# Performance work log

Hardware: AMD Instinct MI355X
Metric: run time of the kernel (lower is better)

## Reference

```python
import jax, jax.numpy as jnp
from jax import lax
import numpy as np

MAX_ATOMS = 50
MAX_DEGREE = 4
MAX_RINGS = 16
BATCH = 16384
EDGE_KEEP_PROB = 0.3  # fraction of neighbor slots that are real edges; rest are -1 (masked)


def setup_inputs() -> dict:
    key = jax.random.key(0)
    k1, k2 = jax.random.split(key)
    e = jax.random.randint(k1, (BATCH, MAX_ATOMS, MAX_DEGREE), 0, MAX_ATOMS, dtype=jnp.int32)
    keep = jax.random.uniform(k2, (BATCH, MAX_ATOMS, MAX_DEGREE)) < EDGE_KEEP_PROB
    edge = jnp.where(keep, e, jnp.int32(-1))
    return {"edge": edge}


def reference(edge):
    B, A, D = edge.shape
    N = A + 1  # node 0 is the masked-edge sentinel after +1 shift and zero-row pad
    bidx = jnp.arange(B)
    # masked_edges: shift indices by +1, pad a zero row at atom index 0 -> [B, N, D]
    me = jnp.pad(edge.astype(jnp.int32) + 1, ((0, 0), (1, 0), (0, 0)))

    # per-node state, shape [B, N]
    lnf = jnp.ones((B, N), jnp.int32).at[:, 0].set(0).at[:, 1].set(0)  # leaf_not_found
    nnv = jnp.ones((B, N), jnp.int32).at[:, 0].set(0)                  # node_not_visited
    Tree = jnp.zeros((B, N), jnp.int32)                                 # parent pointers
    num_rings = jnp.zeros((B,), jnp.int32)
    ring_idx = jnp.zeros((B, N, 2), jnp.int32)

    def visit(state, visiting):
        lnf, nnv, Tree, num_rings, ring_idx = state
        for d in range(D):  # small static degree loop (4)
            nxt = me[bidx, visiting, d]                 # [B]
            slnf = lnf[bidx, nxt]                       # specific_leaf_not_found
            slnv = nnv[bidx, nxt]                       # specific_leaf_not_visited
            cyc = (1 - slnf) * slnv * (nxt != 0).astype(jnp.int32)  # cycle_found
            ring_idx = ring_idx.at[bidx, num_rings, 0].add(visiting * cyc)
            ring_idx = ring_idx.at[bidx, num_rings, 1].add(nxt * cyc)
            num_rings = num_rings + cyc
            Tree = Tree.at[bidx, nxt].add(slnf * visiting)
            lnf = lnf.at[bidx, nxt].set(0)
        nnv = nnv.at[bidx, visiting].set(0)
        return (lnf, nnv, Tree, num_rings, ring_idx)

    # atom_idx == 1: visit node 1 (special-cased init above)
    state = visit((lnf, nnv, Tree, num_rings, ring_idx), jnp.ones((B,), jnp.int32))

    def atom_body(_, state):
        lnf, nnv = state[0], state[1]
        visiting = jnp.argmax(nnv * (1 - lnf), axis=-1).astype(jnp.int32)
        return visit(state, visiting)

    state = lax.fori_loop(2, A + 1, atom_body, state)
    lnf, nnv, Tree, num_rings, ring_idx = state

    max_num_rings = jnp.max(num_rings)
    rings = jnp.zeros((B, MAX_RINGS, A), jnp.int32)

    def ring_body(carry):
        i, rings = carry
        air = jnp.zeros((B,), jnp.int32)  # atom_in_ring_idx

        # branch 0: mark ancestor chain of ring endpoint 0
        start = ring_idx[:, i, 0]
        vb0 = jnp.zeros((B, N), jnp.int32).at[bidx, start].set(1)
        def mark0(_, c):
            vb0, start = c
            nxt = Tree[bidx, start]
            return (vb0.at[bidx, nxt].set(1), nxt)
        vb0, _ = lax.fori_loop(0, A, mark0, (vb0, start))

        # branch 1: walk ancestor chain of endpoint 1, emit atoms until chains meet
        start = ring_idx[:, i, 1]
        vb1 = jnp.zeros((B, N), jnp.int32).at[bidx, start].set(1)
        rings = rings.at[bidx, i, air].set(start)
        def b1(_, c):
            rings, vb1, start, air = c
            nxt = Tree[bidx, start]
            same = jnp.any(vb0 * vb1 == 1, axis=-1)
            nsv = (~same).astype(jnp.int32)
            air = air + nsv
            rings = rings.at[bidx, i, air].add(nxt * nsv)
            vb1 = vb1.at[bidx, nxt].set(1)
            return (rings, vb1, nxt, air)
        rings, vb1, _, air = lax.fori_loop(0, A, b1, (rings, vb1, start, air))

        # branch 2: walk endpoint-0 chain again, emit atoms until it meets branch 1
        start = ring_idx[:, i, 0]
        vb0b = jnp.zeros((B, N), jnp.int32).at[bidx, start].set(1)
        air = air + 1
        rings = rings.at[bidx, i, air].set(start)
        def b2(_, c):
            rings, vb0b, start, air = c
            nxt = Tree[bidx, start]
            vb0b = vb0b.at[bidx, nxt].set(1)
            same = jnp.any(vb0b * vb1 == 1, axis=-1)
            nsv = (~same).astype(jnp.int32)
            air = air + nsv
            rings = rings.at[bidx, i, air].add(nxt * nsv)
            return (rings, vb0b, nxt, air)
        rings, _, _, _ = lax.fori_loop(0, A, b2, (rings, vb0b, start, air))
        return (i + 1, rings)

    def ring_cond(carry):
        return carry[0] < max_num_rings

    _, rings = lax.while_loop(ring_cond, ring_body, (jnp.int32(0), rings))
    return (Tree, ring_idx, rings - 1)
```

## Files before the change

### kernel.cpp

```cpp
#include <hip/hip_runtime.h>
#include <stdint.h>

constexpr int BATCH = 16384;
constexpr int A     = 50;
constexpr int NN    = 51;
constexpr int MAXR  = 16;
constexpr int EPB   = 16;
constexpr int EPWB  = 4;
constexpr int WPB   = 4;

__device__ __forceinline__ void prep_row(int lane, int dep,
    int s0lo, int s0hi, int s1lo, int s1hi, int pack, int i,
    int& pos, int& ta, int& tua, int& s0v)
{
    const uint64_t s0 = ((uint64_t)(uint32_t)__builtin_amdgcn_readlane(s0hi, i) << 32)
                      |  (uint32_t)__builtin_amdgcn_readlane(s0lo, i);
    const uint64_t s1 = ((uint64_t)(uint32_t)__builtin_amdgcn_readlane(s1hi, i) << 32)
                      |  (uint32_t)__builtin_amdgcn_readlane(s1lo, i);
    const int pk = __builtin_amdgcn_readlane(pack, i);
    const int dm = pk & 0xff, ds0 = (pk >> 8) & 0xff, ds1 = (pk >> 16) & 0xff;
    s0v = (pk >> 24) & 0xff;
    ta  = ds1 - dm;
    tua = ta + ds0 - dm;
    const bool on1 = ((s1 >> lane) & 1) && (dep >= dm);
    const bool on0 = ((s0 >> lane) & 1) && (dep >  dm);
    int p = on1 ? (ds1 - dep) : on0 ? (ta + 1 + ds0 - dep) : 63;
    pos = p < 63 ? p : 63;
}

__global__ __launch_bounds__(WPB * 64, 4)
void fused_kernel(const int* __restrict__ edge, int* __restrict__ out)
{
    const int tid   = threadIdx.x;
    const int bbase = blockIdx.x * EPB;

    __shared__ uint32_t eds [EPB][NN];
    __shared__ uint16_t comb[EPB][128];

    {
        ((uint4*)&comb[0][0])[tid] = make_uint4(0, 0, 0, 0);
    }
    {
        const int4* e4 = (const int4*)edge + (size_t)bbase * A;
        #pragma unroll
        for (int k = 0; k < 4; ++k) {
            const int gi = k * 256 + tid;
            if (gi < EPB * A) {
                const int4 v = e4[gi];
                const int el = gi / A, n = gi - A * el;
                eds[el][n] = (uint32_t)(v.x + 1) | ((uint32_t)(v.y + 1) << 8)
                           | ((uint32_t)(v.z + 1) << 16) | ((uint32_t)(v.w + 1) << 24);
            }
        }
    }
    __syncthreads();

    if (tid < 64) {
        const int e = tid >> 2;
        const int d = tid & 3;

        uint64_t L = (((uint64_t)1 << NN) - 1) & ~(uint64_t)3;
        uint64_t V = (((uint64_t)1 << NN) - 1) & ~(uint64_t)1;
        uint64_t M = 2;
        int visiting = 1, nr = 0;
        uint32_t w = eds[e][0];

        #pragma unroll 1
        for (int it = 0; it < A; ++it) {
            const int n0 = w & 0xff, n1 = (w >> 8) & 0xff, n2 = (w >> 16) & 0xff, n3 = w >> 24;
            const uint64_t bu = ((uint64_t)1 << n0) | ((uint64_t)1 << n1)
                              | ((uint64_t)1 << n2) | ((uint64_t)1 << n3);
            const int myn = (w >> (8 * d)) & 0xff;
            const uint64_t bm = (uint64_t)1 << myn;
            const uint64_t visbit = (uint64_t)1 << visiting;
            const uint64_t Mn = (M | (V & bu)) & ~visbit;
            const bool dn = (Mn == 0);
            const uint64_t Msafe = dn ? (uint64_t)2 : Mn;
            const int nv = (int)__builtin_ctzll(Msafe);
            const uint32_t wn = eds[e][nv - 1];
            const bool dup = ((d > 0) & (myn == n0)) | ((d > 1) & (myn == n1)) | ((d > 2) & (myn == n2));
            const bool fa  = ((L & bm) == 0) | dup;
            const bool cf  = fa & ((V & bm) != 0) & (myn != 0);
            const uint64_t Bc = __ballot(cf);
            const uint32_t qb = (uint32_t)(Bc >> (tid & 60)) & 0xfu;
            const int slot = nr + __builtin_popcount(qb & ((1u << d) - 1));
            nr += __builtin_popcount(qb);
            if (!fa) comb[e][myn] = (uint16_t)visiting;
            if (cf && slot < NN)
                comb[e][64 + slot] = (uint16_t)(visiting | (myn << 8));
            L &= ~bu;
            V &= ~visbit;
            M = Mn; visiting = nv;
            w = dn ? 0u : wn;
            if (__ballot(!dn) == 0) break;
        }
    }
    __syncthreads();

    const int lane  = tid & 63;
    const int wid   = tid >> 6;
    const int ebase = wid * EPWB;
    const int gbase = bbase + ebase;

    int*  otree = out;
    int2* oridx = (int2*)(out + (size_t)BATCH * NN);

    uint64_t MkE[EPWB];
    int gE[EPWB], r01E[EPWB];
    #pragma unroll
    for (int j = 0; j < EPWB; ++j) {
        const int ew = ebase + j;
        const int b  = gbase + j;
        const int f = (lane < NN) ? (int)comb[ew][lane] : 0;
        const uint32_t pv = (lane < NN) ? (uint32_t)comb[ew][64 + lane] : 0;
        MkE[j] = ((uint64_t)1 << lane) | ((uint64_t)1 << f);
        gE[j]  = f;
        r01E[j] = (int)pv;
        if (lane < NN) {
            otree[(size_t)b * NN + lane] = f;
            oridx[(size_t)b * NN + lane] = make_int2((int)(pv & 0xff), (int)(pv >> 8));
        }
    }
    #pragma unroll
    for (int j6 = 0; j6 < 6; ++j6) {
        int lo4[EPWB], hi4[EPWB], gg4[EPWB];
        #pragma unroll
        for (int j = 0; j < EPWB; ++j) {
            const int ad = gE[j] << 2;
            lo4[j] = __builtin_amdgcn_ds_bpermute(ad, (int)(uint32_t)MkE[j]);
            hi4[j] = __builtin_amdgcn_ds_bpermute(ad, (int)(MkE[j] >> 32));
            gg4[j] = (j6 < 5) ? __builtin_amdgcn_ds_bpermute(ad, gE[j]) : gE[j];
        }
        #pragma unroll
        for (int j = 0; j < EPWB; ++j) {
            MkE[j] |= ((uint64_t)(uint32_t)hi4[j] << 32) | (uint32_t)lo4[j];
            gE[j]   = gg4[j];
        }
    }
    int depE[EPWB], nactE[EPWB], packE[EPWB];
    int s0loE[EPWB], s0hiE[EPWB], s1loE[EPWB], s1hiE[EPWB];
    {
        int t0l[EPWB], t0h[EPWB], t1l[EPWB], t1h[EPWB];
        #pragma unroll
        for (int j = 0; j < EPWB; ++j) {
            const int Mlo = (int)(uint32_t)MkE[j], Mhi = (int)(MkE[j] >> 32);
            const int a0 = (r01E[j] & 0xff) << 2, a1 = ((r01E[j] >> 8) & 0xff) << 2;
            t0l[j] = __builtin_amdgcn_ds_bpermute(a0, Mlo);
            t0h[j] = __builtin_amdgcn_ds_bpermute(a0, Mhi);
            t1l[j] = __builtin_amdgcn_ds_bpermute(a1, Mlo);
            t1h[j] = __builtin_amdgcn_ds_bpermute(a1, Mhi);
        }
        #pragma unroll
        for (int j = 0; j < EPWB; ++j) {
            const uint64_t set0 = ((uint64_t)(uint32_t)t0h[j] << 32) | (uint32_t)t0l[j];
            const uint64_t set1 = ((uint64_t)(uint32_t)t1h[j] << 32) | (uint32_t)t1l[j];
            depE[j] = __builtin_popcountll(MkE[j]) - 1;
            const int dm  = __builtin_popcountll(set0 & set1) - 1;
            const int ds0 = __builtin_popcountll(set0) - 1;
            const int ds1 = __builtin_popcountll(set1) - 1;
            const int r0  = r01E[j] & 0xff;
            s0loE[j] = (int)(uint32_t)set0;  s0hiE[j] = (int)(set0 >> 32);
            s1loE[j] = (int)(uint32_t)set1;  s1hiE[j] = (int)(set1 >> 32);
            packE[j] = dm | (ds0 << 8) | (ds1 << 16) | (r0 << 24);
            nactE[j] = __popcll(__ballot((lane < MAXR) && (r0 != 0)));
        }
    }

    #pragma unroll
    for (int j = 0; j < EPWB; ++j) {
        const int b = gbase + j;
        int* orings = out + (size_t)BATCH * NN * 3 + (size_t)b * (MAXR * A);
        const int nact = nactE[j];
        const int dep  = depE[j];

        int i = 0;
        for (; i + 3 < nact; i += 4) {
            int p0,t0,u0,v0, p1,t1,u1,v1, p2,t2,u2,v2, p3,t3,u3,v3;
            prep_row(lane, dep, s0loE[j], s0hiE[j], s1loE[j], s1hiE[j], packE[j], i+0, p0,t0,u0,v0);
            prep_row(lane, dep, s0loE[j], s0hiE[j], s1loE[j], s1hiE[j], packE[j], i+1, p1,t1,u1,v1);
            prep_row(lane, dep, s0loE[j], s0hiE[j], s1loE[j], s1hiE[j], packE[j], i+2, p2,t2,u2,v2);
            prep_row(lane, dep, s0loE[j], s0hiE[j], s1loE[j], s1hiE[j], packE[j], i+3, p3,t3,u3,v3);
            const int m0 = __builtin_amdgcn_ds_permute(p0 << 2, lane);
            const int m1 = __builtin_amdgcn_ds_permute(p1 << 2, lane);
            const int m2 = __builtin_amdgcn_ds_permute(p2 << 2, lane);
            const int m3 = __builtin_amdgcn_ds_permute(p3 << 2, lane);
            const int r0v = (lane == t0 + 1) ? v0 : (lane <= u0 ? m0 : 0);
            const int r1v = (lane == t1 + 1) ? v1 : (lane <= u1 ? m1 : 0);
            const int r2v = (lane == t2 + 1) ? v2 : (lane <= u2 ? m2 : 0);
            const int r3v = (lane == t3 + 1) ? v3 : (lane <= u3 ? m3 : 0);
            if (lane < A) {
                orings[(i + 0) * A + lane] = r0v - 1;
                orings[(i + 1) * A + lane] = r1v - 1;
                orings[(i + 2) * A + lane] = r2v - 1;
                orings[(i + 3) * A + lane] = r3v - 1;
            }
        }
        for (; i < nact; ++i) {
            int p0, t0, u0, v0;
            prep_row(lane, dep, s0loE[j], s0hiE[j], s1loE[j], s1hiE[j], packE[j], i, p0,t0,u0,v0);
            const int m0 = __builtin_amdgcn_ds_permute(p0 << 2, lane);
            const int r0v = (lane == t0 + 1) ? v0 : (lane <= u0 ? m0 : 0);
            if (lane < A) orings[i * A + lane] = r0v - 1;
        }
        const int startw = nact * A;
        int2* p2w = (int2*)(orings + startw);
        const int n2 = (MAXR * A - startw) >> 1;
        for (int k = lane; k < n2; k += 64) p2w[k] = make_int2(-1, -1);
    }
}

extern "C" void kernel_launch(void* const* d_in, const int* in_sizes, int n_in,
                              void* d_out, int out_size, void* d_ws, size_t ws_size,
                              hipStream_t stream) {
    const int* edge = (const int*)d_in[0];
    int* out = (int*)d_out;
    hipLaunchKernelGGL(fused_kernel, dim3(BATCH / EPB), dim3(WPB * 64), 0, stream,
                       edge, out);
}
```

Measured before the change: 26.88 us.

## Stage ring rows in shared memory via scatter, then store with int4

Ring output rows are no longer built with ds_permute gathers and written directly to global memory as scalar stores. Each warp fills a per-warp shared buffer with -1, scatters each lane's atom to its ring position, and copies the whole 800-int block to global memory using int4 vector stores. The intent is fully coalesced 16-byte global writes in place of masked 4-byte row stores plus a separate fill loop. In exchange it adds about 12.8 KB of shared memory per block, which may limit occupancy, and adds extra LDS traffic. It also relies on ordering within a wavefront without an explicit barrier.

```diff
diff --git a/kernel.cpp b/kernel.cpp
--- a/kernel.cpp
+++ b/kernel.cpp
@@ -8,25 +8,8 @@
 constexpr int EPB   = 16;
 constexpr int EPWB  = 4;
 constexpr int WPB   = 4;
-
-__device__ __forceinline__ void prep_row(int lane, int dep,
-    int s0lo, int s0hi, int s1lo, int s1hi, int pack, int i,
-    int& pos, int& ta, int& tua, int& s0v)
-{
-    const uint64_t s0 = ((uint64_t)(uint32_t)__builtin_amdgcn_readlane(s0hi, i) << 32)
-                      |  (uint32_t)__builtin_amdgcn_readlane(s0lo, i);
-    const uint64_t s1 = ((uint64_t)(uint32_t)__builtin_amdgcn_readlane(s1hi, i) << 32)
-                      |  (uint32_t)__builtin_amdgcn_readlane(s1lo, i);
-    const int pk = __builtin_amdgcn_readlane(pack, i);
-    const int dm = pk & 0xff, ds0 = (pk >> 8) & 0xff, ds1 = (pk >> 16) & 0xff;
-    s0v = (pk >> 24) & 0xff;
-    ta  = ds1 - dm;
-    tua = ta + ds0 - dm;
-    const bool on1 = ((s1 >> lane) & 1) && (dep >= dm);
-    const bool on0 = ((s0 >> lane) & 1) && (dep >  dm);
-    int p = on1 ? (ds1 - dep) : on0 ? (ta + 1 + ds0 - dep) : 63;
-    pos = p < 63 ? p : 63;
-}
+constexpr int RW    = MAXR * A;
+constexpr int RW4   = RW / 4;
 
 __global__ __launch_bounds__(WPB * 64, 4)
 void fused_kernel(const int* __restrict__ edge, int* __restrict__ out)
@@ -36,6 +19,7 @@
 
     __shared__ uint32_t eds [EPB][NN];
     __shared__ uint16_t comb[EPB][128];
+    __shared__ int      rbuf[WPB][RW];
 
     {
         ((uint4*)&comb[0][0])[tid] = make_uint4(0, 0, 0, 0);
@@ -166,46 +150,41 @@
         }
     }
 
-    #pragma unroll
+    int4* rb4 = (int4*)&rbuf[wid][0];
+    #pragma unroll 1
     for (int j = 0; j < EPWB; ++j) {
         const int b = gbase + j;
-        int* orings = out + (size_t)BATCH * NN * 3 + (size_t)b * (MAXR * A);
         const int nact = nactE[j];
         const int dep  = depE[j];
 
-        int i = 0;
-        for (; i + 3 < nact; i += 4) {
-            int p0,t0,u0,v0, p1,t1,u1,v1, p2,t2,u2,v2, p3,t3,u3,v3;
-            prep_row(lane, dep, s0loE[j], s0hiE[j], s1loE[j], s1hiE[j], packE[j], i+0, p0,t0,u0,v0);
-            prep_row(lane, dep, s0loE[j], s0hiE[j], s1loE[j], s1hiE[j], packE[j], i+1, p1,t1,u1,v1);
-            prep_row(lane, dep, s0loE[j], s0hiE[j], s1loE[j], s1hiE[j], packE[j], i+2, p2,t2,u2,v2);
-            prep_row(lane, dep, s0loE[j], s0hiE[j], s1loE[j], s1hiE[j], packE[j], i+3, p3,t3,u3,v3);
-            const int m0 = __builtin_amdgcn_ds_permute(p0 << 2, lane);
-            const int m1 = __builtin_amdgcn_ds_permute(p1 << 2, lane);
-            const int m2 = __builtin_amdgcn_ds_permute(p2 << 2, lane);
-            const int m3 = __builtin_amdgcn_ds_permute(p3 << 2, lane);
-            const int r0v = (lane == t0 + 1) ? v0 : (lane <= u0 ? m0 : 0);
-            const int r1v = (lane == t1 + 1) ? v1 : (lane <= u1 ? m1 : 0);
-            const int r2v = (lane == t2 + 1) ? v2 : (lane <= u2 ? m2 : 0);
-            const int r3v = (lane == t3 + 1) ? v3 : (lane <= u3 ? m3 : 0);
-            if (lane < A) {
-                orings[(i + 0) * A + lane] = r0v - 1;
-                orings[(i + 1) * A + lane] = r1v - 1;
-                orings[(i + 2) * A + lane] = r2v - 1;
-                orings[(i + 3) * A + lane] = r3v - 1;
-            }
+        const int4 m1 = make_int4(-1, -1, -1, -1);
+        #pragma unroll
+        for (int k = 0; k < 4; ++k) {
+            const int f = k * 64 + lane;
+            if (f < RW4) rb4[f] = m1;
         }
-        for (; i < nact; ++i) {
-            int p0, t0, u0, v0;
-            prep_row(lane, dep, s0loE[j], s0hiE[j], s1loE[j], s1hiE[j], packE[j], i, p0,t0,u0,v0);
-            const int m0 = __builtin_amdgcn_ds_permute(p0 << 2, lane);
-            const int r0v = (lane == t0 + 1) ? v0 : (lane <= u0 ? m0 : 0);
-            if (lane < A) orings[i * A + lane] = r0v - 1;
+        for (int i = 0; i < nact; ++i) {
+            const uint64_t s0 = ((uint64_t)(uint32_t)__builtin_amdgcn_readlane(s0hiE[j], i) << 32)
+                              |  (uint32_t)__builtin_amdgcn_readlane(s0loE[j], i);
+            const uint64_t s1 = ((uint64_t)(uint32_t)__builtin_amdgcn_readlane(s1hiE[j], i) << 32)
+                              |  (uint32_t)__builtin_amdgcn_readlane(s1loE[j], i);
+            const int pk = __builtin_amdgcn_readlane(packE[j], i);
+            const int dm = pk & 0xff, ds0 = (pk >> 8) & 0xff, ds1 = (pk >> 16) & 0xff;
+            const int s0v = (pk >> 24) & 0xff;
+            const int ta = ds1 - dm;
+            const bool on1 = ((s1 >> lane) & 1) && (dep >= dm);
+            const bool on0 = ((s0 >> lane) & 1) && (dep >  dm);
+            const int pos = on1 ? (ds1 - dep) : on0 ? (ta + 1 + ds0 - dep) : 99;
+            if (pos < A) rbuf[wid][i * A + pos] = lane - 1;
+            if (lane == 63 && ta + 1 < A)
+                rbuf[wid][i * A + ta + 1] = s0v - 1;
         }
-        const int startw = nact * A;
-        int2* p2w = (int2*)(orings + startw);
-        const int n2 = (MAXR * A - startw) >> 1;
-        for (int k = lane; k < n2; k += 64) p2w[k] = make_int2(-1, -1);
+        int4* og = (int4*)(out + (size_t)BATCH * NN * 3 + (size_t)b * RW);
+        #pragma unroll
+        for (int k = 0; k < 4; ++k) {
+            const int f = k * 64 + lane;
+            if (f < RW4) og[f] = rb4[f];
+        }
     }
 }
 
```

Result: no change. 26.68 us (-0.7%).

## Split fused kernel into separate tree-build and ring-extraction kernels

Applied to the files above, without the earlier changes.

Splits the single fused kernel into two launches. The first is a one-wave tree kernel that runs the serial BFS walk and writes the Tree and ring_idx outputs. The second is a rings kernel that reads those outputs back from global memory and handles two molecules per wave instead of four, with higher occupancy. The aim is to stop three idle waves waiting at a barrier while one wave does the serial traversal, and to spread ring extraction across more waves. In exchange it adds a second launch and a global-memory round trip for the intermediate results.

```diff
diff --git a/kernel.cpp b/kernel.cpp
--- a/kernel.cpp
+++ b/kernel.cpp
@@ -6,8 +6,96 @@
 constexpr int NN    = 51;
 constexpr int MAXR  = 16;
 constexpr int EPB   = 16;
-constexpr int EPWB  = 4;
-constexpr int WPB   = 4;
+constexpr int EPWB  = 2;
+constexpr int WPB2  = 4;
+
+__global__ __launch_bounds__(64)
+void tree_kernel(const int* __restrict__ edge, int* __restrict__ out)
+{
+    const int lane  = threadIdx.x;
+    const int bbase = blockIdx.x * EPB;
+
+    __shared__ uint32_t eds [EPB][NN];
+    __shared__ uint16_t comb[EPB][128];
+
+    {
+        uint4* c16 = (uint4*)&comb[0][0];
+        #pragma unroll
+        for (int k = 0; k < 4; ++k) c16[k * 64 + lane] = make_uint4(0, 0, 0, 0);
+    }
+    {
+        const int4* e4 = (const int4*)edge + (size_t)bbase * A;
+        #pragma unroll
+        for (int k = 0; k < 13; ++k) {
+            const int gi = k * 64 + lane;
+            if (gi < EPB * A) {
+                const int4 v = e4[gi];
+                const int el = gi / A, n = gi - A * el;
+                eds[el][n] = (uint32_t)(v.x + 1) | ((uint32_t)(v.y + 1) << 8)
+                           | ((uint32_t)(v.z + 1) << 16) | ((uint32_t)(v.w + 1) << 24);
+            }
+        }
+    }
+
+    const int e = lane >> 2;
+    const int d = lane & 3;
+
+    uint64_t L = (((uint64_t)1 << NN) - 1) & ~(uint64_t)3;
+    uint64_t V = (((uint64_t)1 << NN) - 1) & ~(uint64_t)1;
+    uint64_t M = 2;
+    int visiting = 1, nr = 0;
+    uint32_t w = eds[e][0];
+
+    #pragma unroll 1
+    for (int it = 0; it < A; ++it) {
+        const int n0 = w & 0xff, n1 = (w >> 8) & 0xff, n2 = (w >> 16) & 0xff, n3 = w >> 24;
+        const uint64_t bu = ((uint64_t)1 << n0) | ((uint64_t)1 << n1)
+                          | ((uint64_t)1 << n2) | ((uint64_t)1 << n3);
+        const int myn = (w >> (8 * d)) & 0xff;
+        const uint64_t bm = (uint64_t)1 << myn;
+        const uint64_t visbit = (uint64_t)1 << visiting;
+        const uint64_t Mn = (M | (V & bu)) & ~visbit;
+        const bool dn = (Mn == 0);
+        const uint64_t Msafe = dn ? (uint64_t)2 : Mn;
+        const int nv = (int)__builtin_ctzll(Msafe);
+        const uint32_t wn = eds[e][nv - 1];
+        const bool dup = ((d > 0) & (myn == n0)) | ((d > 1) & (myn == n1)) | ((d > 2) & (myn == n2));
+        const bool fa  = ((L & bm) == 0) | dup;
+        const bool cf  = fa & ((V & bm) != 0) & (myn != 0);
+        const uint64_t Bc = __ballot(cf);
+        const uint32_t qb = (uint32_t)(Bc >> (lane & 60)) & 0xfu;
+        const int slot = nr + __builtin_popcount(qb & ((1u << d) - 1));
+        nr += __builtin_popcount(qb);
+        if (!fa) comb[e][myn] = (uint16_t)visiting;
+        if (cf && slot < NN)
+            comb[e][64 + slot] = (uint16_t)(visiting | (myn << 8));
+        L &= ~bu;
+        V &= ~visbit;
+        M = Mn; visiting = nv;
+        w = dn ? 0u : wn;
+        if (__ballot(!dn) == 0) break;
+    }
+
+    int* otree = out + (size_t)bbase * NN;
+    #pragma unroll
+    for (int k = 0; k < 13; ++k) {
+        const int fi = k * 64 + lane;
+        if (fi < EPB * NN) {
+            const int el = fi / NN, n = fi - NN * el;
+            otree[fi] = (int)comb[el][n];
+        }
+    }
+    int2* oridx = (int2*)(out + (size_t)BATCH * NN) + (size_t)bbase * NN;
+    #pragma unroll
+    for (int k = 0; k < 13; ++k) {
+        const int fi = k * 64 + lane;
+        if (fi < EPB * NN) {
+            const int el = fi / NN, i = fi - NN * el;
+            const uint32_t pv = comb[el][64 + i];
+            oridx[fi] = make_int2((int)(pv & 0xff), (int)(pv >> 8));
+        }
+    }
+}
 
 __device__ __forceinline__ void prep_row(int lane, int dep,
     int s0lo, int s0hi, int s1lo, int s1hi, int pack, int i,
@@ -28,98 +116,31 @@
     pos = p < 63 ? p : 63;
 }
 
-__global__ __launch_bounds__(WPB * 64, 4)
-void fused_kernel(const int* __restrict__ edge, int* __restrict__ out)
+__global__ __launch_bounds__(WPB2 * 64, 8)
+void rings_kernel(int* __restrict__ out)
 {
     const int tid   = threadIdx.x;
-    const int bbase = blockIdx.x * EPB;
-
-    __shared__ uint32_t eds [EPB][NN];
-    __shared__ uint16_t comb[EPB][128];
-
-    {
-        ((uint4*)&comb[0][0])[tid] = make_uint4(0, 0, 0, 0);
-    }
-    {
-        const int4* e4 = (const int4*)edge + (size_t)bbase * A;
-        #pragma unroll
-        for (int k = 0; k < 4; ++k) {
-            const int gi = k * 256 + tid;
-            if (gi < EPB * A) {
-                const int4 v = e4[gi];
-                const int el = gi / A, n = gi - A * el;
-                eds[el][n] = (uint32_t)(v.x + 1) | ((uint32_t)(v.y + 1) << 8)
-                           | ((uint32_t)(v.z + 1) << 16) | ((uint32_t)(v.w + 1) << 24);
-            }
-        }
-    }
-    __syncthreads();
-
-    if (tid < 64) {
-        const int e = tid >> 2;
-        const int d = tid & 3;
-
-        uint64_t L = (((uint64_t)1 << NN) - 1) & ~(uint64_t)3;
-        uint64_t V = (((uint64_t)1 << NN) - 1) & ~(uint64_t)1;
-        uint64_t M = 2;
-        int visiting = 1, nr = 0;
-        uint32_t w = eds[e][0];
-
-        #pragma unroll 1
-        for (int it = 0; it < A; ++it) {
-            const int n0 = w & 0xff, n1 = (w >> 8) & 0xff, n2 = (w >> 16) & 0xff, n3 = w >> 24;
-            const uint64_t bu = ((uint64_t)1 << n0) | ((uint64_t)1 << n1)
-                              | ((uint64_t)1 << n2) | ((uint64_t)1 << n3);
-            const int myn = (w >> (8 * d)) & 0xff;
-            const uint64_t bm = (uint64_t)1 << myn;
-            const uint64_t visbit = (uint64_t)1 << visiting;
-            const uint64_t Mn = (M | (V & bu)) & ~visbit;
-            const bool dn = (Mn == 0);
-            const uint64_t Msafe = dn ? (uint64_t)2 : Mn;
-            const int nv = (int)__builtin_ctzll(Msafe);
-            const uint32_t wn = eds[e][nv - 1];
-            const bool dup = ((d > 0) & (myn == n0)) | ((d > 1) & (myn == n1)) | ((d > 2) & (myn == n2));
-            const bool fa  = ((L & bm) == 0) | dup;
-            const bool cf  = fa & ((V & bm) != 0) & (myn != 0);
-            const uint64_t Bc = __ballot(cf);
-            const uint32_t qb = (uint32_t)(Bc >> (tid & 60)) & 0xfu;
-            const int slot = nr + __builtin_popcount(qb & ((1u << d) - 1));
-            nr += __builtin_popcount(qb);
-            if (!fa) comb[e][myn] = (uint16_t)visiting;
-            if (cf && slot < NN)
-                comb[e][64 + slot] = (uint16_t)(visiting | (myn << 8));
-            L &= ~bu;
-            V &= ~visbit;
-            M = Mn; visiting = nv;
-            w = dn ? 0u : wn;
-            if (__ballot(!dn) == 0) break;
-        }
-    }
-    __syncthreads();
-
     const int lane  = tid & 63;
     const int wid   = tid >> 6;
-    const int ebase = wid * EPWB;
-    const int gbase = bbase + ebase;
-
-    int*  otree = out;
-    int2* oridx = (int2*)(out + (size_t)BATCH * NN);
+    const int gbase = (blockIdx.x * WPB2 + wid) * EPWB;
+
+    const int*  tree_base = out;
+    const int2* ridx_base = (const int2*)(out + (size_t)BATCH * NN);
 
     uint64_t MkE[EPWB];
     int gE[EPWB], r01E[EPWB];
     #pragma unroll
     for (int j = 0; j < EPWB; ++j) {
-        const int ew = ebase + j;
-        const int b  = gbase + j;
-        const int f = (lane < NN) ? (int)comb[ew][lane] : 0;
-        const uint32_t pv = (lane < NN) ? (uint32_t)comb[ew][64 + lane] : 0;
+        const int b = gbase + j;
+        int f = 0, r01 = 0;
+        if (lane < NN) {
+            f = tree_base[(size_t)b * NN + lane];
+            const int2 rid = ridx_base[(size_t)b * NN + lane];
+            r01 = rid.x | (rid.y << 8);
+        }
         MkE[j] = ((uint64_t)1 << lane) | ((uint64_t)1 << f);
         gE[j]  = f;
-        r01E[j] = (int)pv;
-        if (lane < NN) {
-            otree[(size_t)b * NN + lane] = f;
-            oridx[(size_t)b * NN + lane] = make_int2((int)(pv & 0xff), (int)(pv >> 8));
-        }
+        r01E[j] = r01;
     }
     #pragma unroll
     for (int j6 = 0; j6 < 6; ++j6) {
@@ -214,6 +235,6 @@
                               hipStream_t stream) {
     const int* edge = (const int*)d_in[0];
     int* out = (int*)d_out;
-    hipLaunchKernelGGL(fused_kernel, dim3(BATCH / EPB), dim3(WPB * 64), 0, stream,
-                       edge, out);
-}
+    hipLaunchKernelGGL(tree_kernel,  dim3(BATCH / EPB),           dim3(64),        0, stream, edge, out);
+    hipLaunchKernelGGL(rings_kernel, dim3(BATCH / (WPB2 * EPWB)), dim3(WPB2 * 64), 0, stream, out);
+}
```

Result: slower. 37.32 us (+38.9%).
